# Kernel optimization log

Measured on AMD Instinct MI355X. Metric: run time of the kernel, lower is better.

The kernel has to match this reference:

```python
import jax, jax.numpy as jnp
import numpy as np

B, N, NC = 8, 25200, 80           # YOLOv5-640 / COCO raw output
CONF_THRES = 0.25                  # init conf_threshold
IOU_THRES = 0.45                   # init iou_threshold
PATCH_CONF = 0.001                 # hard-coded patch_conf in forward
GN = jnp.array([640.0, 640.0, 640.0, 640.0], dtype=jnp.float32)  # img_size[[1,0,1,0]]
MAX_WH = 4096.0                    # class offset for class-aware NMS
K_CLEAN = 512                      # fixed-size cap on NMS candidates (clean branch)
K_PATCH = 1024                     # fixed-size cap on NMS candidates (patch branch)
MAX_DET_CLEAN = 1000
MAX_DET_PATCH = 30000
NEG = jnp.float32(-1e30)


def _xywh2xyxy(x):
    xy, wh = x[..., :2], x[..., 2:4]
    return jnp.concatenate([xy - wh * 0.5, xy + wh * 0.5], axis=-1)


def _pairwise_iou(a, b):
    # a: [A,4] xyxy, b: [B,4] xyxy -> [A,B] jaccard overlap
    tl = jnp.maximum(a[:, None, :2], b[None, :, :2])
    br = jnp.minimum(a[:, None, 2:4], b[None, :, 2:4])
    wh = jnp.clip(br - tl, 0.0)
    inter = wh[..., 0] * wh[..., 1]
    area_a = (a[:, 2] - a[:, 0]) * (a[:, 3] - a[:, 1])
    area_b = (b[:, 2] - b[:, 0]) * (b[:, 3] - b[:, 1])
    union = area_a[:, None] + area_b[None, :] - inter
    union = jnp.where(union > 0, union, 1.0)  # guard degenerate boxes
    return inter / union


def _nms_single(pred, conf_thres, K, max_det):
    # pred: [N, 5+nc]. Fixed-size (padded/masked) greedy NMS, class-aware via MAX_WH offset.
    obj = pred[:, 4]
    cls_conf = pred[:, 5:] * obj[:, None]          # x[:,5:] *= x[:,4:5]
    conf = jnp.max(cls_conf, axis=-1)
    cls = jnp.argmax(cls_conf, axis=-1)
    box = _xywh2xyxy(pred[:, :4])
    valid = (obj > conf_thres) & (conf > conf_thres)
    scores = jnp.where(valid, conf, NEG)
    top_scores, idx = jax.lax.top_k(scores, K)     # sorted desc, like torchvision NMS ordering
    boxes = box[idx]
    cls_k = cls[idx]
    valid_k = top_scores > conf_thres
    boxes_off = boxes + cls_k.astype(boxes.dtype)[:, None] * MAX_WH
    iou = jax.lax.stop_gradient(_pairwise_iou(boxes_off, boxes_off))
    ar = jnp.arange(K)

    def step(keep, i):
        sup = keep[i] & (iou[i] > IOU_THRES) & (ar > i)
        return keep & (~sup), None

    keep, _ = jax.lax.scan(step, valid_k, jnp.arange(K))
    rank = jnp.cumsum(keep.astype(jnp.int32))
    keep = keep & (rank <= max_det)
    return boxes, cls_k, keep


def _image_loss(cb, cc, ck, pb, pc, pk):
    # per clean detection: max IoU over kept patch boxes of the same class (0 if none)
    iou = _pairwise_iou(cb / GN, pb / GN)          # [K_CLEAN, K_PATCH]
    mask = ck[:, None] & pk[None, :] & (cc[:, None] == pc[None, :])
    tm = jnp.max(jnp.where(mask, iou, 0.0), axis=1)
    s = jnp.sum(jnp.where(ck, tm, 0.0))
    n = jnp.sum(ck.astype(jnp.float32))
    return s, n


def _forward(output_clean, output_patch):
    cb, cc, ck = jax.vmap(lambda p: _nms_single(p, CONF_THRES, K_CLEAN, MAX_DET_CLEAN))(output_clean)
    pb, pc, pk = jax.vmap(lambda p: _nms_single(p, PATCH_CONF, K_PATCH, MAX_DET_PATCH))(output_patch)
    s, n = jax.vmap(_image_loss)(cb, cc, ck, pb, pc, pk)
    total, cnt = jnp.sum(s), jnp.sum(n)
    return jnp.where(cnt > 0, 1.0 - total / jnp.maximum(cnt, 1.0), jnp.float32(1.0))


def _make_pred(key):
    ka, kb, kc, kd = jax.random.split(key, 4)
    cxcy = jax.random.uniform(ka, (B, N, 2), jnp.float32, 20.0, 620.0)
    wh = jax.random.uniform(kb, (B, N, 2), jnp.float32, 2.0, 150.0)
    obj = jax.random.uniform(kc, (B, N, 1), jnp.float32)
    clsp = jax.random.uniform(kd, (B, N, NC), jnp.float32)
    return jnp.concatenate([cxcy, wh, obj, clsp], axis=-1)


def setup_inputs() -> dict:
    key = jax.random.key(0)
    k1, k2 = jax.random.split(key)
    return {"output_clean": _make_pred(k1), "output_patch": _make_pred(k2)}


def reference(output_clean, output_patch):
    return _forward(output_clean, output_patch)
```

## Files before the change

### kernel.cpp

```cpp
#include <hip/hip_runtime.h>


static constexpr int NB   = 8;
static constexpr int NA   = 25200;
static constexpr int NCLS = 80;
static constexpr int CH   = 85;
static constexpr int NT   = 16;
static constexpr int KMAX = 1024;
static constexpr int NBIN = 32768;
static constexpr int PSH  = 17;
static constexpr int CAP  = 2048;
static constexpr int IOB  = 34;

static constexpr size_t OFF_KEYS = 0;
static constexpr size_t OFF_CLS  = OFF_KEYS + (size_t)NT * NA * 4;
static constexpr size_t OFF_BOX  = OFF_CLS  + (size_t)NT * NA * 4;
static constexpr size_t OFF_CLSK = OFF_BOX  + (size_t)NT * KMAX * 16;
static constexpr size_t OFF_VALK = OFF_CLSK + (size_t)NT * KMAX * 4;
static constexpr size_t OFF_KEEP = OFF_VALK + (size_t)NT * KMAX * 4;
static constexpr size_t OFF_SUP  = OFF_KEEP + (size_t)NT * 16 * 8;
static constexpr size_t OFF_DIAG = OFF_SUP  + (size_t)NT * KMAX * 16 * 8;
static constexpr size_t OFF_PART = OFF_DIAG + (size_t)NT * KMAX * 8;
static constexpr size_t OFF_CNT  = OFF_PART + 512;

__device__ __forceinline__ unsigned okey(float f) {
  unsigned u = __float_as_uint(f);
  return (u & 0x80000000u) ? ~u : (u | 0x80000000u);
}

__device__ __forceinline__ unsigned long long shflx64(unsigned long long v, int m) {
  unsigned lo = (unsigned)v, hi = (unsigned)(v >> 32);
  lo = __shfl_xor(lo, m);
  hi = __shfl_xor(hi, m);
  return ((unsigned long long)hi << 32) | lo;
}

__global__ __launch_bounds__(256) void k_score(const float* __restrict__ clean,
                                               const float* __restrict__ patch,
                                               unsigned* __restrict__ keys,
                                               int* __restrict__ clsArr,
                                               unsigned* __restrict__ cnt) {
#pragma clang fp contract(off)
  if (blockIdx.x == 0 && blockIdx.y == 0 && threadIdx.x == 0) *cnt = 0u;
  __shared__ float rows[4][32 * CH];
  const int t    = blockIdx.y;
  const int wave = threadIdx.x >> 6;
  const int lane = threadIdx.x & 63;
  const int a0   = blockIdx.x * 128 + wave * 32;
  if (a0 >= NA) return;
  const int nA = (NA - a0 < 32) ? (NA - a0) : 32;
  const float conf_th = (t < 8) ? 0.25f : 0.001f;
  const float* __restrict__ src = ((t < 8) ? clean : patch) + (size_t)(t & 7) * NA * CH;
  const float4* g4 = (const float4*)(src + (size_t)a0 * CH);
  float4* rows4 = (float4*)rows[wave];
  const int n4 = (nA * CH) >> 2;
#pragma unroll
  for (int c = 0; c < 11; ++c) {
    const int i = (c << 6) + lane;
    if (i < n4) {
      __builtin_amdgcn_global_load_lds(
          (const __attribute__((address_space(1))) void*)(g4 + i),
          (__attribute__((address_space(3))) void*)(rows4 + (c << 6)),
          16, 0, 2 );
    }
  }
  asm volatile("s_waitcnt vmcnt(0)" ::: "memory");
  __builtin_amdgcn_sched_barrier(0);

  const int ar = lane >> 1;
  const int q  = lane & 1;
  if (ar < nA) {
    const float* r = rows[wave] + ar * CH;
    const float obj = r[4];
    const int c0 = q * 40;
    float best = r[5 + c0] * obj;
    int bc = c0;
    for (int c = c0 + 1; c < c0 + 40; ++c) {
      float v = r[5 + c] * obj;
      if (v > best) { best = v; bc = c; }
    }
    float b1 = __shfl_down(best, 1); int c1 = __shfl_down(bc, 1);
    if (b1 > best || (b1 == best && c1 < bc)) { best = b1; bc = c1; }
    if (q == 0) {
      const bool valid = (obj > conf_th) && (best > conf_th);
      const float score = valid ? best : -1e30f;
      const int a = a0 + ar;
      keys[(size_t)t * NA + a]   = okey(score);
      clsArr[(size_t)t * NA + a] = bc;
    }
  }
}

__global__ __launch_bounds__(1024) void k_topsel(const unsigned* __restrict__ keys,
                                                 const int* __restrict__ clsArr,
                                                 const float* __restrict__ clean,
                                                 const float* __restrict__ patch,
                                                 float* __restrict__ boxesK,
                                                 int* __restrict__ clsK,
                                                 int* __restrict__ validK) {
#pragma clang fp contract(off)
  const int t = blockIdx.x;
  const unsigned K = (t < 8) ? 512u : 1024u;
  const float conf_th = (t < 8) ? 0.25f : 0.001f;
  __shared__ unsigned h32[NBIN / 2];
  __shared__ unsigned long long buf[CAP];
  __shared__ unsigned scnt[2];
  __shared__ unsigned wtot[16], wsuf[16];
  __shared__ int s_chunk;
  __shared__ unsigned s_acc, s_B;
  const int tid = threadIdx.x;
  const int lane = tid & 63, wv = tid >> 6;
  for (int i = tid; i < NBIN / 2; i += 1024) h32[i] = 0u;
  for (int i = tid; i < CAP; i += 1024) buf[i] = 0ull;
  if (tid < 2) scnt[tid] = 0u;
  __syncthreads();
  const unsigned INVKEY = okey(-1e30f);
  const unsigned* kv = keys + (size_t)t * NA;
  {
    const uint4* kv4 = (const uint4*)kv;
    unsigned invCnt = 0;
    for (int i = tid; i < NA / 4; i += 1024) {
      uint4 kq = kv4[i];
      unsigned kk[4] = {kq.x, kq.y, kq.z, kq.w};
#pragma unroll
      for (int c = 0; c < 4; ++c) {
        if (kk[c] == INVKEY) {
          ++invCnt;
        } else {
          unsigned b = kk[c] >> PSH;
          atomicAdd(&h32[b >> 1], 1u << ((b & 1) * 16));
        }
      }
    }
    for (int off = 32; off > 0; off >>= 1) invCnt += __shfl_down(invCnt, off);
    if (lane == 0 && invCnt) {
      unsigned b = INVKEY >> PSH;
      atomicAdd(&h32[b >> 1], invCnt << ((b & 1) * 16));
    }
  }
  __syncthreads();
  unsigned cnt_c = 0;
  for (int i = 0; i < 16; ++i) {
    unsigned v = h32[tid * 16 + i];
    cnt_c += (v & 0xFFFFu) + (v >> 16);
  }
  unsigned s = cnt_c;
  for (int off = 1; off < 64; off <<= 1) {
    unsigned v = __shfl_down(s, off);
    if (lane + off < 64) s += v;
  }
  if (lane == 0) wtot[wv] = s;
  __syncthreads();
  if (tid < 16) {
    unsigned acc = 0;
    for (int w2 = 15; w2 > tid; --w2) acc += wtot[w2];
    wsuf[tid] = acc;
  }
  __syncthreads();
  const unsigned suf = s + wsuf[wv];
  if (suf >= K && suf - cnt_c < K) { s_chunk = tid; s_acc = suf - cnt_c; }
  __syncthreads();
  if (tid == 0) {
    unsigned acc = s_acc;
    unsigned res = (unsigned)(s_chunk * 32);
    for (int i = 31; i >= 0; --i) {
      int bb = s_chunk * 32 + i;
      unsigned v = h32[bb >> 1];
      unsigned c2 = (bb & 1) ? (v >> 16) : (v & 0xFFFFu);
      if (acc + c2 >= K) { res = (unsigned)bb; break; }
      acc += c2;
    }
    s_B = res;
  }
  __syncthreads();
  const unsigned B = s_B;
  const unsigned long long lowmask =
      (lane == 0) ? 0ull : (0xFFFFFFFFFFFFFFFFull >> (64 - lane));
  for (int i = tid; i < 25600; i += 1024) {
    const bool inb = (i < NA);
    unsigned key = inb ? kv[i] : 0u;
    unsigned p = key >> PSH;
    const bool hi = inb && (p > B);
    const bool eq = inb && (p == B);
    const unsigned long long item =
        ((unsigned long long)key << 32) | (unsigned)(~(unsigned)i);
    unsigned long long mh = __ballot(hi);
    if (mh) {
      int leader = (int)__ffsll(mh) - 1;
      unsigned base2 = 0;
      if (lane == leader) base2 = atomicAdd(&scnt[0], (unsigned)__popcll(mh));
      base2 = __shfl(base2, leader);
      if (hi) {
        unsigned pos = base2 + (unsigned)__popcll(mh & lowmask);
        if (pos < 1024u) buf[pos] = item;
      }
    }
    unsigned long long me = __ballot(eq);
    if (me) {
      int leader = (int)__ffsll(me) - 1;
      unsigned base2 = 0;
      if (lane == leader) base2 = atomicAdd(&scnt[1], (unsigned)__popcll(me));
      base2 = __shfl(base2, leader);
      if (eq) {
        unsigned pos = base2 + (unsigned)__popcll(me & lowmask);
        if (pos < 1024u) buf[1024 + pos] = item;
      }
    }
  }
  __syncthreads();
  {
    const int e0 = wv * 128 + lane;
    const int e1 = e0 + 64;
    unsigned long long r0 = buf[e0], r1 = buf[e1];
    for (int kk2 = 2; kk2 <= CAP; kk2 <<= 1) {
      for (int j = kk2 >> 1; j > 0; j >>= 1) {
        if (j >= 128) {
          buf[e0] = r0; buf[e1] = r1;
          __syncthreads();
          unsigned long long o0 = buf[e0 ^ j];
          unsigned long long o1 = buf[e1 ^ j];
          const bool mx = (((e0 & kk2) == 0) == ((e0 & j) == 0));
          r0 = mx ? (r0 > o0 ? r0 : o0) : (r0 < o0 ? r0 : o0);
          r1 = mx ? (r1 > o1 ? r1 : o1) : (r1 < o1 ? r1 : o1);
          __syncthreads();
        } else if (j == 64) {
          const bool up = (e0 & kk2) == 0;
          unsigned long long mxv = r0 > r1 ? r0 : r1;
          unsigned long long mnv = r0 > r1 ? r1 : r0;
          r0 = up ? mxv : mnv;
          r1 = up ? mnv : mxv;
        } else {
          unsigned long long o0 = shflx64(r0, j);
          unsigned long long o1 = shflx64(r1, j);
          const bool up0 = (e0 & kk2) == 0;
          const bool up1 = (e1 & kk2) == 0;
          const bool lo  = (lane & j) == 0;
          const bool m0 = (up0 == lo), m1 = (up1 == lo);
          r0 = m0 ? (r0 > o0 ? r0 : o0) : (r0 < o0 ? r0 : o0);
          r1 = m1 ? (r1 > o1 ? r1 : o1) : (r1 < o1 ? r1 : o1);
        }
      }
    }
    buf[e0] = r0; buf[e1] = r1;
  }
  __syncthreads();
  const float* __restrict__ src = ((t < 8) ? clean : patch) + (size_t)(t & 7) * NA * CH;
  const unsigned vkey = okey(conf_th);
  for (int k = tid; k < (int)K; k += 1024) {
    unsigned long long v = buf[k];
    unsigned key = (unsigned)(v >> 32);
    int idx = (int)(~(unsigned)(v & 0xFFFFFFFFull));
    if (idx < 0 || idx >= NA) idx = 0;
    const float* r = src + (size_t)idx * CH;
    float cx = r[0], cy = r[1], w = r[2], h = r[3];
    float hw = w * 0.5f, hh = h * 0.5f;
    float* bo = boxesK + ((size_t)t * KMAX + k) * 4;
    bo[0] = cx - hw; bo[1] = cy - hh; bo[2] = cx + hw; bo[3] = cy + hh;
    clsK[t * KMAX + k]   = clsArr[(size_t)t * NA + idx];
    validK[t * KMAX + k] = (key > vkey) ? 1 : 0;
  }
}

__global__ __launch_bounds__(256) void k_ioumat(const float* __restrict__ boxesK,
                                                const int* __restrict__ clsK,
                                                unsigned long long* __restrict__ sup,
                                                unsigned long long* __restrict__ diag) {
#pragma clang fp contract(off)
  const int t  = blockIdx.y;
  const int K  = (t < 8) ? 512 : 1024;
  const int lw = (t < 8) ? 3 : 4;
  const int nw = 1 << lw;
  const int npair = (nw * (nw + 1)) / 2;
  const int total = npair * 64;
  if (blockIdx.x * 256 >= total) return;
  __shared__ float X1[KMAX + 16], Y1[KMAX + 16], X2[KMAX + 16], Y2[KMAX + 16], AR[KMAX + 16];
  for (int i = threadIdx.x; i < K; i += 256) {
    const float* bo = boxesK + ((size_t)t * KMAX + i) * 4;
    float off = (float)clsK[t * KMAX + i] * 4096.0f;
    float x1 = bo[0] + off, y1 = bo[1] + off, x2 = bo[2] + off, y2 = bo[3] + off;
    const int ip = i + (i >> 6);
    X1[ip] = x1; Y1[ip] = y1; X2[ip] = x2; Y2[ip] = y2;
    AR[ip] = (x2 - x1) * (y2 - y1);
  }
  __syncthreads();
  unsigned long long* supt = sup + (size_t)t * (KMAX * 16);
  for (int widx = blockIdx.x * 256 + threadIdx.x; widx < total; widx += IOB * 256) {
    int p = widx >> 6;
    int row = widx & 63;
    int rb = 0, pr = p;
    while (pr >= nw - rb) { pr -= nw - rb; ++rb; }
    const int wc = rb + pr;
    const int i = rb * 64 + row;
    const int ipi = i + rb;
    const float x1i = X1[ipi], y1i = Y1[ipi], x2i = X2[ipi], y2i = Y2[ipi], ai = AR[ipi];
    unsigned long long m = 0ull;
    const int jb = (wc << 6) + wc;
    const bool offd = (wc > rb);
#pragma unroll 4
    for (int l = 0; l < 64; ++l) {
      const int jp = jb + l;
      float tlx = fmaxf(x1i, X1[jp]);
      float tly = fmaxf(y1i, Y1[jp]);
      float brx = fminf(x2i, X2[jp]);
      float bry = fminf(y2i, Y2[jp]);
      float w = fmaxf(brx - tlx, 0.0f);
      float h = fmaxf(bry - tly, 0.0f);
      float inter = w * h;
      float uni = (ai + AR[jp]) - inter;
      uni = (uni > 0.0f) ? uni : 1.0f;
      float iou = inter / uni;
      bool hit = (iou > 0.45f) && (offd || ((wc << 6) + l > i));
      m |= hit ? (1ull << l) : 0ull;
    }
    supt[(size_t)i * nw + wc] = m;
    if (wc == rb) diag[(size_t)t * KMAX + i] = m;
  }
}

template <int LW>
__device__ __forceinline__ void greedy_body(const unsigned long long* __restrict__ sup,
                                            const unsigned long long* __restrict__ diag,
                                            const int* __restrict__ validK,
                                            unsigned long long* __restrict__ keepw,
                                            int t, unsigned long long* sdiag,
                                            unsigned long long* bufLDS) {
  constexpr int NW = 1 << LW;
  constexpr int K  = NW * 64;
  constexpr int CHUNKS = NW / 2;
  constexpr int BLKU64 = 64 * NW;
  const int lane = threadIdx.x;
  const unsigned long long* base = sup + (size_t)t * (KMAX * 16);
  {
    const char* blk0 = (const char*)base;
#pragma unroll
    for (int c = 0; c < CHUNKS; ++c) {
      __builtin_amdgcn_global_load_lds(
          (const __attribute__((address_space(1))) void*)(blk0 + (size_t)(c * 64 + lane) * 16),
          (__attribute__((address_space(3))) void*)((char*)bufLDS + c * 1024),
          16, 0, 0);
    }
  }
  const unsigned long long* dg = diag + (size_t)t * KMAX;
  for (int i = lane; i < K; i += 64) sdiag[i] = dg[i];
  int v16[NW];
#pragma unroll
  for (int W = 0; W < NW; ++W) v16[W] = validK[t * KMAX + W * 64 + lane];
  unsigned long long vkeep = 0ull;
#pragma unroll
  for (int W = 0; W < NW; ++W) {
    unsigned long long bl = __ballot(v16[W] != 0);
    if (lane == W) vkeep = bl;
  }
  asm volatile("s_waitcnt vmcnt(0)" ::: "memory");
  __builtin_amdgcn_sched_barrier(0);

  const int w  = lane & (NW - 1);
  const int b  = lane >> LW;
  const int r0 = b * NW;
  unsigned long long remv = 0ull;
  unsigned long long curs[NW];
#pragma unroll
  for (int W = 0; W < NW; ++W) {
    if (W + 1 < NW) {
      const char* blkn = (const char*)(base + (size_t)(W + 1) * BLKU64);
      char* dst = (char*)(bufLDS + ((W + 1) & 1) * BLKU64);
#pragma unroll
      for (int c = 0; c < CHUNKS; ++c) {
        __builtin_amdgcn_global_load_lds(
            (const __attribute__((address_space(1))) void*)(blkn + (size_t)(c * 64 + lane) * 16),
            (__attribute__((address_space(3))) void*)(dst + c * 1024),
            16, 0, 0);
      }
    }
    unsigned long long cur = __shfl(vkeep, W) & ~__shfl(remv, W);
    for (int rb = 0; rb < 64; rb += 16) {
      unsigned long long tm[16];
#pragma unroll
      for (int i2 = 0; i2 < 16; ++i2) tm[i2] = sdiag[W * 64 + rb + i2];
#pragma unroll
      for (int i2 = 0; i2 < 16; ++i2) {
        unsigned long long msk = 0ull - ((cur >> (rb + i2)) & 1ull);
        cur &= ~(tm[i2] & msk);
      }
    }
    curs[W] = cur;
    if (W + 1 < NW) {
      if constexpr (NW == 16) { asm volatile("s_waitcnt vmcnt(8)" ::: "memory"); }
      else                    { asm volatile("s_waitcnt vmcnt(4)" ::: "memory"); }
      __builtin_amdgcn_sched_barrier(0);
      const unsigned long long* bw = bufLDS + (W & 1) * BLKU64;
      unsigned long long part = 0ull;
#pragma unroll
      for (int j = 0; j < NW; ++j) {
        unsigned long long v = bw[(r0 + j) * NW + w];
        bool take = (w > W) && ((cur >> (r0 + j)) & 1ull);
        part |= take ? v : 0ull;
      }
      for (int s = NW; s < 64; s <<= 1) part |= __shfl_xor(part, s);
      remv |= part;
    }
  }
  if (lane == 0) {
#pragma unroll
    for (int W = 0; W < NW; ++W) keepw[t * 16 + W] = curs[W];
  }
}

__global__ __launch_bounds__(64) void k_greedy(const unsigned long long* __restrict__ sup,
                                               const unsigned long long* __restrict__ diag,
                                               const int* __restrict__ validK,
                                               unsigned long long* __restrict__ keepw) {
  __shared__ unsigned long long sdiag[KMAX];
  __shared__ unsigned long long buf2[2 * 64 * 16];
  const int t = blockIdx.x;
  if (t < 8) greedy_body<3>(sup, diag, validK, keepw, t, sdiag, buf2);
  else       greedy_body<4>(sup, diag, validK, keepw, t, sdiag, buf2);
}

__global__ __launch_bounds__(1024) void k_loss(const float* __restrict__ boxesK,
                                               const int* __restrict__ clsK,
                                               const unsigned long long* __restrict__ keepw,
                                               float* __restrict__ part,
                                               unsigned* __restrict__ cnt,
                                               float* __restrict__ out) {
#pragma clang fp contract(off)
  const int img = blockIdx.y;
  const int chunk = blockIdx.x;
  const int tp = 8 + img;
  __shared__ float px1[KMAX], py1[KMAX], px2[KMAX], py2[KMAX], pa[KMAX];
  __shared__ int pcls[KMAX];
  __shared__ float red[1024];
  __shared__ unsigned s_last;
  for (int j = threadIdx.x; j < KMAX; j += 1024) {
    const float* bo = boxesK + ((size_t)tp * KMAX + j) * 4;
    float x1 = bo[0] / 640.0f, y1 = bo[1] / 640.0f;
    float x2 = bo[2] / 640.0f, y2 = bo[3] / 640.0f;
    px1[j] = x1; py1[j] = y1; px2[j] = x2; py2[j] = y2;
    pa[j] = (x2 - x1) * (y2 - y1);
    int kept = (int)((keepw[tp * 16 + (j >> 6)] >> (j & 63)) & 1ull);
    pcls[j] = kept ? clsK[tp * KMAX + j] : -1;
  }
  __syncthreads();
  const int row = chunk * 64 + (threadIdx.x & 63);
  const int stripe = threadIdx.x >> 6;
  const int ck = (int)((keepw[img * 16 + (row >> 6)] >> (row & 63)) & 1ull);
  const float* bo = boxesK + ((size_t)img * KMAX + row) * 4;
  float cx1 = bo[0] / 640.0f, cy1 = bo[1] / 640.0f;
  float cx2 = bo[2] / 640.0f, cy2 = bo[3] / 640.0f;
  float ca = (cx2 - cx1) * (cy2 - cy1);
  const int ccls = clsK[img * KMAX + row];
  float m = 0.0f;
  if (ck) {
    const int j0 = stripe * 64;
    for (int j = j0; j < j0 + 64; ++j) {
      if (pcls[j] == ccls) {
        float tlx = fmaxf(cx1, px1[j]);
        float tly = fmaxf(cy1, py1[j]);
        float brx = fminf(cx2, px2[j]);
        float bry = fminf(cy2, py2[j]);
        float w = fmaxf(brx - tlx, 0.0f);
        float h = fmaxf(bry - tly, 0.0f);
        float inter = w * h;
        float uni = (ca + pa[j]) - inter;
        uni = (uni > 0.0f) ? uni : 1.0f;
        m = fmaxf(m, inter / uni);
      }
    }
  }
  red[threadIdx.x] = m;
  __syncthreads();
  if (threadIdx.x < 64) {
    float mm = red[threadIdx.x];
#pragma unroll
    for (int s = 1; s < 16; ++s) mm = fmaxf(mm, red[threadIdx.x + 64 * s]);
    float sv = ck ? mm : 0.0f;
    float nv = ck ? 1.0f : 0.0f;
    for (int off = 32; off > 0; off >>= 1) {
      sv += __shfl_down(sv, off);
      nv += __shfl_down(nv, off);
    }
    if (threadIdx.x == 0) {
      int b = img * 8 + chunk;
      part[b * 2 + 0] = sv;
      part[b * 2 + 1] = nv;
      __threadfence();
      unsigned old = atomicAdd(cnt, 1u);
      s_last = (old == 63u) ? 1u : 0u;
    }
  }
  __syncthreads();
  if (s_last && threadIdx.x < 64) {
    __threadfence();
    volatile const float* vp = part;
    float sv = vp[threadIdx.x * 2 + 0];
    float nv = vp[threadIdx.x * 2 + 1];
    for (int off = 32; off > 0; off >>= 1) {
      sv += __shfl_down(sv, off);
      nv += __shfl_down(nv, off);
    }
    if (threadIdx.x == 0) out[0] = (nv > 0.0f) ? (1.0f - sv / fmaxf(nv, 1.0f)) : 1.0f;
  }
}

extern "C" void kernel_launch(void* const* d_in, const int* in_sizes, int n_in,
                              void* d_out, int out_size, void* d_ws, size_t ws_size,
                              hipStream_t stream) {
  const float* clean = (const float*)d_in[0];
  const float* patch = (const float*)d_in[1];
  char* ws = (char*)d_ws;
  unsigned* keys            = (unsigned*)(ws + OFF_KEYS);
  int* clsArr               = (int*)(ws + OFF_CLS);
  float* boxesK             = (float*)(ws + OFF_BOX);
  int* clsK                 = (int*)(ws + OFF_CLSK);
  int* validK               = (int*)(ws + OFF_VALK);
  unsigned long long* keepw = (unsigned long long*)(ws + OFF_KEEP);
  unsigned long long* sup   = (unsigned long long*)(ws + OFF_SUP);
  unsigned long long* diag  = (unsigned long long*)(ws + OFF_DIAG);
  float* part               = (float*)(ws + OFF_PART);
  unsigned* cnt             = (unsigned*)(ws + OFF_CNT);
  float* out                = (float*)d_out;

  k_score  <<<dim3((NA + 127) / 128, NT), 256, 0, stream>>>(clean, patch, keys, clsArr, cnt);
  k_topsel <<<NT, 1024, 0, stream>>>(keys, clsArr, clean, patch, boxesK, clsK, validK);
  k_ioumat <<<dim3(IOB, NT), 256, 0, stream>>>(boxesK, clsK, sup, diag);
  k_greedy <<<NT, 64, 0, stream>>>(sup, diag, validK, keepw);
  k_loss   <<<dim3(8, NB), 1024, 0, stream>>>(boxesK, clsK, keepw, part, cnt, out);
}
```

Before: 255.0 us.

## Replace LDS staging in greedy NMS with direct register loads and uniform reductions

The greedy NMS kernel drops its double-buffered global-to-LDS staging of suppression blocks and diagonal masks. Each lane now loads its suppression words straight into registers, reads the diagonal from global memory as uniform loads, and keeps per-window valid masks as wave-uniform ballots instead of shuffling them. The removed-mask accumulation is made scalar with readfirstlane. This cuts LDS traffic, explicit waitcnt barriers and shuffles on the serial dependency chain. In exchange, global load latency is exposed inside each window iteration with no explicit prefetch ahead, and register pressure rises.

```diff
diff --git a/kernel.cpp b/kernel.cpp
--- a/kernel.cpp
+++ b/kernel.cpp
@@ -32,6 +32,12 @@
   unsigned lo = (unsigned)v, hi = (unsigned)(v >> 32);
   lo = __shfl_xor(lo, m);
   hi = __shfl_xor(hi, m);
+  return ((unsigned long long)hi << 32) | lo;
+}
+
+__device__ __forceinline__ unsigned long long rfl64(unsigned long long v) {
+  unsigned lo = __builtin_amdgcn_readfirstlane((unsigned)v);
+  unsigned hi = __builtin_amdgcn_readfirstlane((unsigned)(v >> 32));
   return ((unsigned long long)hi << 32) | lo;
 }
 
@@ -322,38 +328,15 @@
                                             const unsigned long long* __restrict__ diag,
                                             const int* __restrict__ validK,
                                             unsigned long long* __restrict__ keepw,
-                                            int t, unsigned long long* sdiag,
-                                            unsigned long long* bufLDS) {
+                                            int t) {
   constexpr int NW = 1 << LW;
-  constexpr int K  = NW * 64;
-  constexpr int CHUNKS = NW / 2;
-  constexpr int BLKU64 = 64 * NW;
   const int lane = threadIdx.x;
+  const unsigned long long* dg   = diag + (size_t)t * KMAX;
   const unsigned long long* base = sup + (size_t)t * (KMAX * 16);
-  {
-    const char* blk0 = (const char*)base;
-#pragma unroll
-    for (int c = 0; c < CHUNKS; ++c) {
-      __builtin_amdgcn_global_load_lds(
-          (const __attribute__((address_space(1))) void*)(blk0 + (size_t)(c * 64 + lane) * 16),
-          (__attribute__((address_space(3))) void*)((char*)bufLDS + c * 1024),
-          16, 0, 0);
-    }
-  }
-  const unsigned long long* dg = diag + (size_t)t * KMAX;
-  for (int i = lane; i < K; i += 64) sdiag[i] = dg[i];
-  int v16[NW];
-#pragma unroll
-  for (int W = 0; W < NW; ++W) v16[W] = validK[t * KMAX + W * 64 + lane];
-  unsigned long long vkeep = 0ull;
-#pragma unroll
-  for (int W = 0; W < NW; ++W) {
-    unsigned long long bl = __ballot(v16[W] != 0);
-    if (lane == W) vkeep = bl;
-  }
-  asm volatile("s_waitcnt vmcnt(0)" ::: "memory");
-  __builtin_amdgcn_sched_barrier(0);
-
+  unsigned long long vk[NW];
+#pragma unroll
+  for (int W = 0; W < NW; ++W)
+    vk[W] = __ballot(validK[t * KMAX + W * 64 + lane] != 0);
   const int w  = lane & (NW - 1);
   const int b  = lane >> LW;
   const int r0 = b * NW;
@@ -361,43 +344,34 @@
   unsigned long long curs[NW];
 #pragma unroll
   for (int W = 0; W < NW; ++W) {
+    unsigned long long vv[NW];
     if (W + 1 < NW) {
-      const char* blkn = (const char*)(base + (size_t)(W + 1) * BLKU64);
-      char* dst = (char*)(bufLDS + ((W + 1) & 1) * BLKU64);
-#pragma unroll
-      for (int c = 0; c < CHUNKS; ++c) {
-        __builtin_amdgcn_global_load_lds(
-            (const __attribute__((address_space(1))) void*)(blkn + (size_t)(c * 64 + lane) * 16),
-            (__attribute__((address_space(3))) void*)(dst + c * 1024),
-            16, 0, 0);
-      }
-    }
-    unsigned long long cur = __shfl(vkeep, W) & ~__shfl(remv, W);
+#pragma unroll
+      for (int j = 0; j < NW; ++j)
+        vv[j] = base[(size_t)(W * 64 + r0 + j) * NW + w];
+    }
+    unsigned long long cur = vk[W] & ~remv;
+#pragma unroll
     for (int rb = 0; rb < 64; rb += 16) {
       unsigned long long tm[16];
 #pragma unroll
-      for (int i2 = 0; i2 < 16; ++i2) tm[i2] = sdiag[W * 64 + rb + i2];
+      for (int i2 = 0; i2 < 16; ++i2) tm[i2] = dg[W * 64 + rb + i2];
 #pragma unroll
       for (int i2 = 0; i2 < 16; ++i2) {
-        unsigned long long msk = 0ull - ((cur >> (rb + i2)) & 1ull);
-        cur &= ~(tm[i2] & msk);
+        unsigned long long tmm = ((cur >> (rb + i2)) & 1ull) ? tm[i2] : 0ull;
+        cur &= ~tmm;
       }
     }
     curs[W] = cur;
     if (W + 1 < NW) {
-      if constexpr (NW == 16) { asm volatile("s_waitcnt vmcnt(8)" ::: "memory"); }
-      else                    { asm volatile("s_waitcnt vmcnt(4)" ::: "memory"); }
-      __builtin_amdgcn_sched_barrier(0);
-      const unsigned long long* bw = bufLDS + (W & 1) * BLKU64;
       unsigned long long part = 0ull;
 #pragma unroll
       for (int j = 0; j < NW; ++j) {
-        unsigned long long v = bw[(r0 + j) * NW + w];
         bool take = (w > W) && ((cur >> (r0 + j)) & 1ull);
-        part |= take ? v : 0ull;
+        part |= take ? vv[j] : 0ull;
       }
       for (int s = NW; s < 64; s <<= 1) part |= __shfl_xor(part, s);
-      remv |= part;
+      remv |= rfl64(part);
     }
   }
   if (lane == 0) {
@@ -410,11 +384,9 @@
                                                const unsigned long long* __restrict__ diag,
                                                const int* __restrict__ validK,
                                                unsigned long long* __restrict__ keepw) {
-  __shared__ unsigned long long sdiag[KMAX];
-  __shared__ unsigned long long buf2[2 * 64 * 16];
   const int t = blockIdx.x;
-  if (t < 8) greedy_body<3>(sup, diag, validK, keepw, t, sdiag, buf2);
-  else       greedy_body<4>(sup, diag, validK, keepw, t, sdiag, buf2);
+  if (t < 8) greedy_body<3>(sup, diag, validK, keepw, t);
+  else       greedy_body<4>(sup, diag, validK, keepw, t);
 }
 
 __global__ __launch_bounds__(1024) void k_loss(const float* __restrict__ boxesK,
```

Result: slower. 263.1 us (+3.2%).
